# Performance work log

Hardware: AMD Instinct MI355X
Metric: run time of the kernel (lower is better)

## Reference

```python
import jax, jax.numpy as jnp
import numpy as np

D_MODEL = 1024
N_HEADS = 16
HEAD_DIM = D_MODEL // N_HEADS
LENGTHS = np.array([1536, 1024, 1400, 900, 1200, 1300, 1500, 1000])
OFFSETS = np.concatenate([[0], np.cumsum(LENGTHS)]).astype(np.int32)
N_TOT = int(OFFSETS[-1])
LN_EPS = 1e-5


def _pad_meta(offsets):
    # Static (numpy) gather indices: ragged concat [N,D] -> padded [B,Lmax,D]
    offsets = np.asarray(offsets)
    lengths = np.diff(offsets)
    lmax = int(lengths.max())
    tok = np.arange(lmax)[None, :]                      # [1, Lmax]
    valid = tok < lengths[:, None]                      # [B, Lmax] bool
    src = np.where(valid, offsets[:-1, None] + tok, 0)  # [B, Lmax] int
    return src, valid


def setup_inputs() -> dict:
    key = jax.random.key(0)
    ks = jax.random.split(key, 4)
    s = 1.0 / np.sqrt(D_MODEL)
    return {
        "x": jax.random.normal(ks[0], (N_TOT, D_MODEL), jnp.float32),
        "batch_offsets": jnp.asarray(OFFSETS, jnp.int32),
        "in_proj_w": jax.random.normal(ks[1], (3 * D_MODEL, D_MODEL), jnp.float32) * s,
        "in_proj_b": jnp.zeros((3 * D_MODEL,), jnp.float32),
        "out_w": jax.random.normal(ks[2], (D_MODEL, D_MODEL), jnp.float32) * s,
        "out_b": jnp.zeros((D_MODEL,), jnp.float32),
        "ln_g": jnp.ones((D_MODEL,), jnp.float32),
        "ln_b": jnp.zeros((D_MODEL,), jnp.float32),
    }


def reference(x, batch_offsets, in_proj_w, in_proj_b, out_w, out_b, ln_g, ln_b):
    src, valid = _pad_meta(np.asarray(batch_offsets))
    B, L = valid.shape
    vmask = jnp.asarray(valid)
    # deconcat_add_batch_dim: pad to [B, L, D]
    xp = x[src] * vmask[..., None]
    # pre-LayerNorm
    mu = jnp.mean(xp, axis=-1, keepdims=True)
    var = jnp.mean((xp - mu) ** 2, axis=-1, keepdims=True)
    h = (xp - mu) * jax.lax.rsqrt(var + LN_EPS) * ln_g + ln_b
    # fused qkv projection (torch MHA in_proj)
    qkv = h @ in_proj_w.T + in_proj_b                   # [B, L, 3D]
    q, k, v = jnp.split(qkv, 3, axis=-1)
    def heads(t):
        return t.reshape(B, L, N_HEADS, HEAD_DIM).transpose(0, 2, 1, 3)
    q, k, v = heads(q), heads(k), heads(v)              # [B, H, L, hd]
    scores = jnp.einsum("bhqd,bhkd->bhqk", q, k) / np.sqrt(HEAD_DIM)
    scores = jnp.where(vmask[:, None, None, :], scores, -jnp.inf)
    attn = jax.nn.softmax(scores, axis=-1)
    o = jnp.einsum("bhqk,bhkd->bhqd", attn, v)          # [B, H, L, hd]
    o = o.transpose(0, 2, 1, 3).reshape(B, L, D_MODEL)
    o = o @ out_w.T + out_b
    y = xp + o                                          # residual (dropout p=0)
    # remove_batch_dim_and_concat: unpad back to [N, D]
    return y[vmask]
```

## Files before the change

kernel.cpp:

```cpp
#include <hip/hip_runtime.h>
#include <hip/hip_bf16.h>
#include <stdint.h>

#define D_MODEL 1024
#define QKV_LD  3072
#define N_TOT   9860
#define M_PAD   9984
#define LN_EPS  1e-5f

typedef __bf16 bf16_t;
typedef __bf16 bf16x8 __attribute__((ext_vector_type(8)));
typedef float  f32x4  __attribute__((ext_vector_type(4)));
typedef float  f32x16 __attribute__((ext_vector_type(16)));
typedef uint32_t u32x4 __attribute__((ext_vector_type(4)));

__device__ inline unsigned short f2bf(float f) {
  __bf16 h = (__bf16)f;
  return __builtin_bit_cast(unsigned short, h);
}
__device__ inline int imin(int a, int b) { return a < b ? a : b; }

__device__ inline void plswap(uint32_t& a, uint32_t& b) {
  asm("v_permlane32_swap_b32 %0, %1" : "+v"(a), "+v"(b));
}

__device__ inline void gload_lds16(const bf16_t* g, void* l) {
  __builtin_amdgcn_global_load_lds(
      (const __attribute__((address_space(1))) unsigned int*)g,
      (__attribute__((address_space(3))) unsigned int*)l, 16, 0, 0);
}

__global__ __launch_bounds__(256) void cvt_weights(const float* __restrict__ w_in,
                                                   const float* __restrict__ w_out,
                                                   bf16_t* __restrict__ win,
                                                   bf16_t* __restrict__ wout) {
  const int n_in = QKV_LD * D_MODEL / 4;
  int i = blockIdx.x * 256 + threadIdx.x;
  const float* src;
  ushort4* dst;
  int j;
  if (i < n_in) { src = w_in; dst = (ushort4*)win; j = i; }
  else          { src = w_out; dst = (ushort4*)wout; j = i - n_in; }
  float4 v = ((const float4*)src)[j];
  dst[j] = make_ushort4(f2bf(v.x), f2bf(v.y), f2bf(v.z), f2bf(v.w));
}

__global__ __launch_bounds__(256) void ln_kernel(const float* __restrict__ x,
                                                 const float* __restrict__ g,
                                                 const float* __restrict__ b,
                                                 bf16_t* __restrict__ hout) {
  int row = blockIdx.x;
  int t = threadIdx.x;
  if (row >= N_TOT) {
    ((ushort4*)(hout + (size_t)row * D_MODEL))[t] = make_ushort4(0, 0, 0, 0);
    return;
  }
  float4 v = ((const float4*)(x + (size_t)row * D_MODEL))[t];
  float s  = v.x + v.y + v.z + v.w;
  float sq = v.x * v.x + v.y * v.y + v.z * v.z + v.w * v.w;
  #pragma unroll
  for (int off = 1; off < 64; off <<= 1) {
    s  += __shfl_xor(s, off);
    sq += __shfl_xor(sq, off);
  }
  __shared__ float ss[4], ssq[4];
  int wid = t >> 6;
  if ((t & 63) == 0) { ss[wid] = s; ssq[wid] = sq; }
  __syncthreads();
  s  = ss[0] + ss[1] + ss[2] + ss[3];
  sq = ssq[0] + ssq[1] + ssq[2] + ssq[3];
  float mu  = s * (1.0f / 1024.0f);
  float var = sq * (1.0f / 1024.0f) - mu * mu;
  float rs  = rsqrtf(var + LN_EPS);
  float4 gv = ((const float4*)g)[t];
  float4 bv = ((const float4*)b)[t];
  ushort4 o;
  o.x = f2bf((v.x - mu) * rs * gv.x + bv.x);
  o.y = f2bf((v.y - mu) * rs * gv.y + bv.y);
  o.z = f2bf((v.z - mu) * rs * gv.z + bv.z);
  o.w = f2bf((v.w - mu) * rs * gv.w + bv.w);
  ((ushort4*)(hout + (size_t)row * D_MODEL))[t] = o;
}

template<int NCOLS>
__global__ __launch_bounds__(512) void gemm256(const bf16_t* __restrict__ A,
                                               const bf16_t* __restrict__ B,
                                               const float* __restrict__ bias,
                                               bf16_t* __restrict__ Cbf) {
  constexpr int K = 1024, NKT = K / 64;
  constexpr int GX = M_PAD / 256;
  constexpr int NWG = GX * (NCOLS / 256);
  int bid = blockIdx.x;
  {
    constexpr int q = NWG / 8, r = NWG % 8;
    int x = bid & 7, o = bid >> 3;
    bid = (x < r ? x * (q + 1) : r * (q + 1) + (x - r) * q) + o;
  }
  const int tileM = bid % GX;
  const int tileN = bid / GX;
  const int t = threadIdx.x;
  const int lane = t & 63, wid = t >> 6;
  const int wr = wid >> 2, wc = wid & 3;

  __shared__ bf16_t As[2][256 * 64];
  __shared__ bf16_t Bs[2][256 * 64];

  f32x4 acc[8][4];
  #pragma unroll
  for (int m = 0; m < 8; ++m)
    #pragma unroll
    for (int n = 0; n < 4; ++n)
      acc[m][n] = f32x4{0.f, 0.f, 0.f, 0.f};

  const int rowA0 = tileM * 256, rowB0 = tileN * 256;
  const int lrow = lane >> 3;
  const int lch  = lane & 7;

  auto stage = [&](int buf, int kt) {
    const int k0 = kt * 64;
    #pragma unroll
    for (int i = 0; i < 4; ++i) {
      const int r  = wid * 32 + i * 8 + lrow;
      const int sc = lch ^ (r & 7);
      gload_lds16(A + (size_t)(rowA0 + r) * K + k0 + sc * 8,
                  (char*)&As[buf][(wid * 32 + i * 8) * 64]);
      gload_lds16(B + (size_t)(rowB0 + r) * K + k0 + sc * 8,
                  (char*)&Bs[buf][(wid * 32 + i * 8) * 64]);
    }
  };

  stage(0, 0);

  for (int kt = 0; kt < NKT; ++kt) {
    const int cur = kt & 1;
    if (kt + 1 < NKT) {
      stage(cur ^ 1, kt + 1);
      asm volatile("s_waitcnt vmcnt(8)" ::: "memory");
    } else {
      asm volatile("s_waitcnt vmcnt(0)" ::: "memory");
    }
    __builtin_amdgcn_s_barrier();
    __builtin_amdgcn_sched_barrier(0);

    const char* Ab = (const char*)&As[cur][0];
    const char* Bb = (const char*)&Bs[cur][0];

    bf16x8 bfr[4][2];
    #pragma unroll
    for (int n = 0; n < 4; ++n)
      #pragma unroll
      for (int ks = 0; ks < 2; ++ks) {
        int r = wc * 64 + n * 16 + (lane & 15);
        int c = ks * 4 + (lane >> 4);
        bfr[n][ks] = *(const bf16x8*)(Bb + r * 128 + ((c ^ (r & 7)) * 16));
      }
    #pragma unroll
    for (int p = 0; p < 4; ++p) {
      bf16x8 af[2][2];
      #pragma unroll
      for (int mm = 0; mm < 2; ++mm)
        #pragma unroll
        for (int ks = 0; ks < 2; ++ks) {
          int r = wr * 128 + (p * 2 + mm) * 16 + (lane & 15);
          int c = ks * 4 + (lane >> 4);
          af[mm][ks] = *(const bf16x8*)(Ab + r * 128 + ((c ^ (r & 7)) * 16));
        }
      __builtin_amdgcn_s_setprio(1);
      #pragma unroll
      for (int mm = 0; mm < 2; ++mm)
        #pragma unroll
        for (int n = 0; n < 4; ++n)
          #pragma unroll
          for (int ks = 0; ks < 2; ++ks)
            acc[p * 2 + mm][n] =
                __builtin_amdgcn_mfma_f32_16x16x32_bf16(af[mm][ks], bfr[n][ks],
                                                        acc[p * 2 + mm][n], 0, 0, 0);
      __builtin_amdgcn_s_setprio(0);
    }
    __builtin_amdgcn_sched_barrier(0);
    __builtin_amdgcn_s_barrier();
  }

  #pragma unroll
  for (int m = 0; m < 8; ++m) {
    int rb = tileM * 256 + wr * 128 + m * 16 + ((lane >> 4) << 2);
    #pragma unroll
    for (int n = 0; n < 4; ++n) {
      int cb = tileN * 256 + wc * 64 + n * 16 + (lane & 15);
      float bv = bias[cb];
      #pragma unroll
      for (int j = 0; j < 4; ++j)
        Cbf[(size_t)(rb + j) * NCOLS + cb] = (bf16_t)(acc[m][n][j] + bv);
    }
  }
}

template<int NCOLS, bool FINAL>
__global__ __launch_bounds__(256) void gemm_bt(const bf16_t* __restrict__ A,
                                               const bf16_t* __restrict__ B,
                                               const float* __restrict__ bias,
                                               bf16_t* __restrict__ Cbf,
                                               float* __restrict__ Cf,
                                               const float* __restrict__ resid) {
  constexpr int K = 1024;
  constexpr int GX = M_PAD / 128;
  constexpr int NWG = GX * (NCOLS / 128);
  int bid = blockIdx.x;
  bid = (bid & 7) * (NWG / 8) + (bid >> 3);
  const int tileM = bid % GX;
  const int tileN = bid / GX;
  const int t = threadIdx.x;
  const int lane = t & 63, wid = t >> 6;
  const int wr = wid >> 1, wc = wid & 1;

  __shared__ bf16_t Asm[128 * 64];
  __shared__ bf16_t Bsm[128 * 64];

  f32x4 acc[4][4];
  #pragma unroll
  for (int m = 0; m < 4; ++m)
    #pragma unroll
    for (int n = 0; n < 4; ++n)
      acc[m][n] = f32x4{0.f, 0.f, 0.f, 0.f};

  const int rowA0 = tileM * 128, rowB0 = tileN * 128;
  const int lrow = lane >> 3;
  const int lch  = lane & 7;

  for (int kt = 0; kt < K / 64; ++kt) {
    __syncthreads();
    const int k0 = kt * 64;
    #pragma unroll
    for (int i = 0; i < 4; ++i) {
      const int r  = wid * 32 + i * 8 + lrow;
      const int sc = lch ^ (r & 7);
      gload_lds16(A + (size_t)(rowA0 + r) * K + k0 + sc * 8,
                  (char*)Asm + (wid * 32 + i * 8) * 128);
      gload_lds16(B + (size_t)(rowB0 + r) * K + k0 + sc * 8,
                  (char*)Bsm + (wid * 32 + i * 8) * 128);
    }
    __syncthreads();
    #pragma unroll
    for (int ks = 0; ks < 2; ++ks) {
      bf16x8 af[4], bfr[4];
      #pragma unroll
      for (int m = 0; m < 4; ++m) {
        int r = wr * 64 + m * 16 + (lane & 15);
        int c = ks * 4 + (lane >> 4);
        af[m] = *(const bf16x8*)((const char*)Asm + r * 128 + ((c ^ (r & 7)) * 16));
      }
      #pragma unroll
      for (int n = 0; n < 4; ++n) {
        int r = wc * 64 + n * 16 + (lane & 15);
        int c = ks * 4 + (lane >> 4);
        bfr[n] = *(const bf16x8*)((const char*)Bsm + r * 128 + ((c ^ (r & 7)) * 16));
      }
      #pragma unroll
      for (int m = 0; m < 4; ++m)
        #pragma unroll
        for (int n = 0; n < 4; ++n)
          acc[m][n] = __builtin_amdgcn_mfma_f32_16x16x32_bf16(af[m], bfr[n], acc[m][n], 0, 0, 0);
    }
  }

  #pragma unroll
  for (int m = 0; m < 4; ++m) {
    int rb = tileM * 128 + wr * 64 + m * 16 + ((lane >> 4) << 2);
    #pragma unroll
    for (int n = 0; n < 4; ++n) {
      int cb = tileN * 128 + wc * 64 + n * 16 + (lane & 15);
      float bv = bias[cb];
      #pragma unroll
      for (int j = 0; j < 4; ++j) {
        int grow = rb + j;
        float val = acc[m][n][j] + bv;
        if constexpr (FINAL) {
          if (grow < N_TOT) {
            size_t idx = (size_t)grow * NCOLS + cb;
            Cf[idx] = resid[idx] + val;
          }
        } else {
          Cbf[(size_t)grow * NCOLS + cb] = (bf16_t)val;
        }
      }
    }
  }
}

__global__ __launch_bounds__(256) void transpose_v(const bf16_t* __restrict__ qkv,
                                                   bf16_t* __restrict__ vt) {
  static const int OFF_[8] = {0, 1536, 2560, 3960, 4860, 6060, 7360, 8860};
  static const int SH_[8]  = {0, 0, 0, 0, 4, 4, 8, 12};
  __shared__ bf16_t tile[64][72];
  const int t = threadIdx.x;
  const int n0 = blockIdx.x * 64, c0 = blockIdx.y * 64;
  #pragma unroll
  for (int it = 0; it < 2; ++it) {
    int idx = it * 256 + t;
    int row = idx >> 3, ch = idx & 7;
    bf16x8 v = *(const bf16x8*)(qkv + (size_t)(n0 + row) * QKV_LD + 2048 + c0 + ch * 8);
    *(bf16x8*)(&tile[row][ch * 8]) = v;
  }
  __syncthreads();
  #pragma unroll
  for (int it = 0; it < 2; ++it) {
    int idx = it * 256 + t;
    int crow = idx >> 3, ng = idx & 7;
    int tok0 = n0 + ng * 8;
    if (tok0 >= N_TOT) continue;
    bf16x8 o;
    #pragma unroll
    for (int i = 0; i < 8; ++i) o[i] = tile[ng * 8 + i][crow];
    int b0 = 0;
    #pragma unroll
    for (int i = 1; i < 8; ++i) b0 += (tok0 >= OFF_[i]);
    bool fast = (tok0 + 7 < N_TOT);
    if (fast) {
      int b7 = 0;
      #pragma unroll
      for (int i = 1; i < 8; ++i) b7 += (tok0 + 7 >= OFF_[i]);
      fast = (b7 == b0);
    }
    bf16_t* vrow = vt + (size_t)(c0 + crow) * M_PAD;
    if (fast) {
      *(bf16x8*)(vrow + tok0 + SH_[b0]) = o;
    } else {
      #pragma unroll
      for (int i = 0; i < 8; ++i) {
        int tok = tok0 + i;
        if (tok < N_TOT) {
          int bb = 0;
          #pragma unroll
          for (int k = 1; k < 8; ++k) bb += (tok >= OFF_[k]);
          vrow[tok + SH_[bb]] = o[i];
        }
      }
    }
  }
}

__global__ __launch_bounds__(256) void attn_mfma(const bf16_t* __restrict__ qkv,
                                                 const bf16_t* __restrict__ vt,
                                                 bf16_t* __restrict__ obuf) {
  static const int off0_[8] = {0, 7360, 2560, 6060, 4860, 1536, 8860, 3960};
  static const int vcol_[8] = {0, 7368, 2560, 6064, 4864, 1536, 8872, 3960};
  static const int len_[8]  = {1536, 1500, 1400, 1300, 1200, 1024, 1000, 900};
  static const int ts_[9]   = {0, 12, 24, 35, 46, 56, 64, 72, 80};
  const int tt = blockIdx.x;
  const int h  = blockIdx.y;
  int b = 0;
  #pragma unroll
  for (int i = 1; i < 8; ++i) b += (tt >= ts_[i]);
  const int L     = len_[b];
  const int kbase = off0_[b];
  const int vcol  = vcol_[b];
  const int q0    = (tt - ts_[b]) * 128;
  const int tok0  = kbase + q0;
  const int nq    = imin(L - q0, 128);

  const int t = threadIdx.x;
  const int lane = t & 63, w = t >> 6;
  const int qcol = lane & 31, hi = lane >> 5;

  __shared__ char Ks[3][8192];
  __shared__ char Vs[3][8192];

  const float MSHIFT = 16.0f;

  bf16x8 qf[4];
  {
    const bf16_t* qp = qkv + (size_t)(tok0 + w * 32 + qcol) * QKV_LD + h * 64;
    #pragma unroll
    for (int c = 0; c < 4; ++c) {
      bf16x8 v = *(const bf16x8*)(qp + c * 16 + hi * 8);
      #pragma unroll
      for (int i = 0; i < 8; ++i) v[i] = (__bf16)((float)v[i] * 0.125f);
      qf[c] = v;
    }
  }

  f32x16 accO[2];
  #pragma unroll
  for (int db = 0; db < 2; ++db)
    #pragma unroll
    for (int i = 0; i < 16; ++i) accO[db][i] = 0.f;
  float lsum = 0.f;

  const int srow = w * 8 + (lane >> 3);
  const int sch  = lane & 7;
  const int sc   = sch ^ (srow & 7);

  auto stage = [&](int buf, int kv0) {
    #pragma unroll
    for (int it = 0; it < 2; ++it) {
      int row = srow + it * 32;
      gload_lds16(qkv + (size_t)(kbase + kv0 + row) * QKV_LD + 1024 + h * 64 + sc * 8,
                  &Ks[buf][w * 1024 + it * 4096]);
      gload_lds16(vt + (size_t)(h * 64 + row) * M_PAD + vcol + kv0 + sc * 8,
                  &Vs[buf][w * 1024 + it * 4096]);
    }
  };

  const int nt = (L + 63) >> 6;
  stage(0, 0);
  stage(1, 64);
  int cur = 0;

  for (int ti = 0; ti < nt; ++ti) {
    const int nk = imin(L - ti * 64, 64);
    if (ti + 1 < nt) {
      asm volatile("s_waitcnt vmcnt(4)" ::: "memory");
    } else {
      asm volatile("s_waitcnt vmcnt(0)" ::: "memory");
    }
    __builtin_amdgcn_s_barrier();
    __builtin_amdgcn_sched_barrier(0);
    if (ti + 2 < nt) {
      int nbuf = cur + 2; if (nbuf >= 3) nbuf -= 3;
      stage(nbuf, (ti + 2) * 64);
    }

    const char* Kb = Ks[cur];
    const char* Vb = Vs[cur];

    f32x16 accS[2];
    #pragma unroll
    for (int kb = 0; kb < 2; ++kb)
      #pragma unroll
      for (int i = 0; i < 16; ++i) accS[kb][i] = 0.f;
    __builtin_amdgcn_s_setprio(1);
    #pragma unroll
    for (int kb = 0; kb < 2; ++kb) {
      int key = kb * 32 + qcol;
      #pragma unroll
      for (int c = 0; c < 4; ++c) {
        bf16x8 kf = *(const bf16x8*)(Kb + key * 128 + (((2 * c + hi) ^ (key & 7)) * 16));
        accS[kb] = __builtin_amdgcn_mfma_f32_32x32x16_bf16(kf, qf[c], accS[kb], 0, 0, 0);
      }
    }
    __builtin_amdgcn_s_setprio(0);

    if (nk < 64) {
      #pragma unroll
      for (int kb = 0; kb < 2; ++kb)
        #pragma unroll
        for (int r = 0; r < 16; ++r)
          if (kb * 32 + (r & 3) + 8 * (r >> 2) + 4 * hi >= nk) accS[kb][r] = -INFINITY;
    }

    bf16x8 pb[2][2];
    #pragma unroll
    for (int kb = 0; kb < 2; ++kb) {
      uint32_t G[4][2];
      #pragma unroll
      for (int j = 0; j < 4; ++j) {
        float p0 = __expf(accS[kb][4 * j + 0] - MSHIFT);
        float p1 = __expf(accS[kb][4 * j + 1] - MSHIFT);
        float p2 = __expf(accS[kb][4 * j + 2] - MSHIFT);
        float p3 = __expf(accS[kb][4 * j + 3] - MSHIFT);
        lsum += (p0 + p1) + (p2 + p3);
        G[j][0] = (uint32_t)f2bf(p0) | ((uint32_t)f2bf(p1) << 16);
        G[j][1] = (uint32_t)f2bf(p2) | ((uint32_t)f2bf(p3) << 16);
      }
      #pragma unroll
      for (int c = 0; c < 2; ++c) {
        uint32_t ax = G[2 * c][0], bx = G[2 * c + 1][0];
        uint32_t ay = G[2 * c][1], by = G[2 * c + 1][1];
        plswap(ax, bx);
        plswap(ay, by);
        u32x4 u; u[0] = ax; u[1] = ay; u[2] = bx; u[3] = by;
        pb[kb][c] = __builtin_bit_cast(bf16x8, u);
      }
    }

    __builtin_amdgcn_s_setprio(1);
    #pragma unroll
    for (int kb = 0; kb < 2; ++kb)
      #pragma unroll
      for (int c = 0; c < 2; ++c) {
        int ch = 4 * kb + 2 * c + hi;
        #pragma unroll
        for (int db = 0; db < 2; ++db) {
          int dim = db * 32 + qcol;
          bf16x8 vf = *(const bf16x8*)(Vb + dim * 128 + ((ch ^ (dim & 7)) * 16));
          accO[db] = __builtin_amdgcn_mfma_f32_32x32x16_bf16(vf, pb[kb][c], accO[db], 0, 0, 0);
        }
      }
    __builtin_amdgcn_s_setprio(0);
    cur = (cur == 2) ? 0 : cur + 1;
  }

  float l = lsum + __shfl_xor(lsum, 32);
  const int qlocal = w * 32 + qcol;
  if (qlocal < nq) {
    float inv = 1.f / l;
    bf16_t* op = obuf + (size_t)(tok0 + qlocal) * D_MODEL + h * 64;
    #pragma unroll
    for (int db = 0; db < 2; ++db)
      #pragma unroll
      for (int rr = 0; rr < 4; ++rr) {
        float v0 = accO[db][4 * rr + 0] * inv;
        float v1 = accO[db][4 * rr + 1] * inv;
        float v2 = accO[db][4 * rr + 2] * inv;
        float v3 = accO[db][4 * rr + 3] * inv;
        uint2 u;
        u.x = (uint32_t)f2bf(v0) | ((uint32_t)f2bf(v1) << 16);
        u.y = (uint32_t)f2bf(v2) | ((uint32_t)f2bf(v3) << 16);
        *(uint2*)(op + db * 32 + rr * 8 + hi * 4) = u;
      }
  }
}

extern "C" void kernel_launch(void* const* d_in, const int* in_sizes, int n_in,
                              void* d_out, int out_size, void* d_ws, size_t ws_size,
                              hipStream_t stream) {
  const float* x     = (const float*)d_in[0];
  const float* w_in  = (const float*)d_in[2];
  const float* b_in  = (const float*)d_in[3];
  const float* w_out = (const float*)d_in[4];
  const float* b_out = (const float*)d_in[5];
  const float* ln_g  = (const float*)d_in[6];
  const float* ln_b  = (const float*)d_in[7];
  float* out = (float*)d_out;

  char* ws = (char*)d_ws;
  const size_t SZ_H   = (size_t)M_PAD * D_MODEL * 2;
  const size_t SZ_QKV = (size_t)M_PAD * QKV_LD * 2;
  const size_t SZ_O   = SZ_H;
  const size_t SZ_WIN = (size_t)QKV_LD * D_MODEL * 2;
  const size_t SZ_WO  = (size_t)D_MODEL * D_MODEL * 2;
  if (ws_size < SZ_H + SZ_QKV + SZ_O + SZ_WIN + SZ_WO) return;

  bf16_t* h_bf    = (bf16_t*)ws;
  bf16_t* qkv_bf  = (bf16_t*)(ws + SZ_H);
  bf16_t* o_bf    = (bf16_t*)(ws + SZ_H + SZ_QKV);
  bf16_t* win_bf  = (bf16_t*)(ws + SZ_H + SZ_QKV + SZ_O);
  bf16_t* wout_bf = (bf16_t*)(ws + SZ_H + SZ_QKV + SZ_O + SZ_WIN);

  cvt_weights<<<(QKV_LD * D_MODEL / 4 + D_MODEL * D_MODEL / 4) / 256, 256, 0, stream>>>(
      w_in, w_out, win_bf, wout_bf);

  ln_kernel<<<M_PAD, 256, 0, stream>>>(x, ln_g, ln_b, h_bf);

  gemm256<QKV_LD><<<(M_PAD / 256) * (QKV_LD / 256), 512, 0, stream>>>(
      h_bf, win_bf, b_in, qkv_bf);

  bf16_t* vt = h_bf;
  transpose_v<<<dim3(M_PAD / 64, D_MODEL / 64), 256, 0, stream>>>(qkv_bf, vt);

  attn_mfma<<<dim3(80, 16), 256, 0, stream>>>(qkv_bf, vt, o_bf);

  gemm_bt<D_MODEL, true><<<(M_PAD / 128) * (D_MODEL / 128), 256, 0, stream>>>(
      o_bf, wout_bf, b_out, nullptr, out, x);
}
```

Baseline: 300.9 us.

## Fuse V transpose into QKV GEMM epilogue and merge weight cvt into LN

```diff
diff --git a/kernel.cpp b/kernel.cpp
--- a/kernel.cpp
+++ b/kernel.cpp
@@ -30,27 +30,28 @@
       (__attribute__((address_space(3))) unsigned int*)l, 16, 0, 0);
 }
 
-__global__ __launch_bounds__(256) void cvt_weights(const float* __restrict__ w_in,
-                                                   const float* __restrict__ w_out,
-                                                   bf16_t* __restrict__ win,
-                                                   bf16_t* __restrict__ wout) {
-  const int n_in = QKV_LD * D_MODEL / 4;
-  int i = blockIdx.x * 256 + threadIdx.x;
-  const float* src;
-  ushort4* dst;
-  int j;
-  if (i < n_in) { src = w_in; dst = (ushort4*)win; j = i; }
-  else          { src = w_out; dst = (ushort4*)wout; j = i - n_in; }
-  float4 v = ((const float4*)src)[j];
-  dst[j] = make_ushort4(f2bf(v.x), f2bf(v.y), f2bf(v.z), f2bf(v.w));
-}
-
-__global__ __launch_bounds__(256) void ln_kernel(const float* __restrict__ x,
-                                                 const float* __restrict__ g,
-                                                 const float* __restrict__ b,
-                                                 bf16_t* __restrict__ hout) {
+__global__ __launch_bounds__(256) void ln_cvt_kernel(const float* __restrict__ x,
+                                                     const float* __restrict__ g,
+                                                     const float* __restrict__ b,
+                                                     bf16_t* __restrict__ hout,
+                                                     const float* __restrict__ w_in,
+                                                     const float* __restrict__ w_out,
+                                                     bf16_t* __restrict__ win,
+                                                     bf16_t* __restrict__ wout) {
   int row = blockIdx.x;
   int t = threadIdx.x;
+  if (row >= M_PAD) {
+    const int n_in = QKV_LD * D_MODEL / 4;
+    int i = (row - M_PAD) * 256 + t;
+    const float* src;
+    ushort4* dst;
+    int j;
+    if (i < n_in) { src = w_in; dst = (ushort4*)win; j = i; }
+    else          { src = w_out; dst = (ushort4*)wout; j = i - n_in; }
+    float4 v = ((const float4*)src)[j];
+    dst[j] = make_ushort4(f2bf(v.x), f2bf(v.y), f2bf(v.z), f2bf(v.w));
+    return;
+  }
   if (row >= N_TOT) {
     ((ushort4*)(hout + (size_t)row * D_MODEL))[t] = make_ushort4(0, 0, 0, 0);
     return;
@@ -82,11 +83,12 @@
   ((ushort4*)(hout + (size_t)row * D_MODEL))[t] = o;
 }
 
-template<int NCOLS>
+template<int NCOLS, bool VT>
 __global__ __launch_bounds__(512) void gemm256(const bf16_t* __restrict__ A,
                                                const bf16_t* __restrict__ B,
                                                const float* __restrict__ bias,
-                                               bf16_t* __restrict__ Cbf) {
+                                               bf16_t* __restrict__ Cbf,
+                                               bf16_t* __restrict__ vt) {
   constexpr int K = 1024, NKT = K / 64;
   constexpr int GX = M_PAD / 256;
   constexpr int NWG = GX * (NCOLS / 256);
@@ -181,16 +183,41 @@
     __builtin_amdgcn_s_barrier();
   }
 
-  #pragma unroll
-  for (int m = 0; m < 8; ++m) {
-    int rb = tileM * 256 + wr * 128 + m * 16 + ((lane >> 4) << 2);
-    #pragma unroll
-    for (int n = 0; n < 4; ++n) {
-      int cb = tileN * 256 + wc * 64 + n * 16 + (lane & 15);
-      float bv = bias[cb];
-      #pragma unroll
-      for (int j = 0; j < 4; ++j)
-        Cbf[(size_t)(rb + j) * NCOLS + cb] = (bf16_t)(acc[m][n][j] + bv);
+  if (VT && tileN >= 8) {
+    static const int OFF_[8] = {0, 1536, 2560, 3960, 4860, 6060, 7360, 8860};
+    static const int SH_[8]  = {0, 0, 0, 0, 4, 4, 8, 12};
+    #pragma unroll
+    for (int m = 0; m < 8; ++m) {
+      int rb = tileM * 256 + wr * 128 + m * 16 + ((lane >> 4) << 2);
+      if (rb >= N_TOT) continue;
+      int bb = 0;
+      #pragma unroll
+      for (int i = 1; i < 8; ++i) bb += (rb >= OFF_[i]);
+      int col0 = rb + SH_[bb];
+      #pragma unroll
+      for (int n = 0; n < 4; ++n) {
+        int cb = tileN * 256 + wc * 64 + n * 16 + (lane & 15);
+        float bv = bias[cb];
+        float v0 = acc[m][n][0] + bv, v1 = acc[m][n][1] + bv;
+        float v2 = acc[m][n][2] + bv, v3 = acc[m][n][3] + bv;
+        uint2 u;
+        u.x = (uint32_t)f2bf(v0) | ((uint32_t)f2bf(v1) << 16);
+        u.y = (uint32_t)f2bf(v2) | ((uint32_t)f2bf(v3) << 16);
+        *(uint2*)(vt + (size_t)(cb - 2048) * M_PAD + col0) = u;
+      }
+    }
+  } else {
+    #pragma unroll
+    for (int m = 0; m < 8; ++m) {
+      int rb = tileM * 256 + wr * 128 + m * 16 + ((lane >> 4) << 2);
+      #pragma unroll
+      for (int n = 0; n < 4; ++n) {
+        int cb = tileN * 256 + wc * 64 + n * 16 + (lane & 15);
+        float bv = bias[cb];
+        #pragma unroll
+        for (int j = 0; j < 4; ++j)
+          Cbf[(size_t)(rb + j) * NCOLS + cb] = (bf16_t)(acc[m][n][j] + bv);
+      }
     }
   }
 }
@@ -281,58 +308,6 @@
           }
         } else {
           Cbf[(size_t)grow * NCOLS + cb] = (bf16_t)val;
-        }
-      }
-    }
-  }
-}
-
-__global__ __launch_bounds__(256) void transpose_v(const bf16_t* __restrict__ qkv,
-                                                   bf16_t* __restrict__ vt) {
-  static const int OFF_[8] = {0, 1536, 2560, 3960, 4860, 6060, 7360, 8860};
-  static const int SH_[8]  = {0, 0, 0, 0, 4, 4, 8, 12};
-  __shared__ bf16_t tile[64][72];
-  const int t = threadIdx.x;
-  const int n0 = blockIdx.x * 64, c0 = blockIdx.y * 64;
-  #pragma unroll
-  for (int it = 0; it < 2; ++it) {
-    int idx = it * 256 + t;
-    int row = idx >> 3, ch = idx & 7;
-    bf16x8 v = *(const bf16x8*)(qkv + (size_t)(n0 + row) * QKV_LD + 2048 + c0 + ch * 8);
-    *(bf16x8*)(&tile[row][ch * 8]) = v;
-  }
-  __syncthreads();
-  #pragma unroll
-  for (int it = 0; it < 2; ++it) {
-    int idx = it * 256 + t;
-    int crow = idx >> 3, ng = idx & 7;
-    int tok0 = n0 + ng * 8;
-    if (tok0 >= N_TOT) continue;
-    bf16x8 o;
-    #pragma unroll
-    for (int i = 0; i < 8; ++i) o[i] = tile[ng * 8 + i][crow];
-    int b0 = 0;
-    #pragma unroll
-    for (int i = 1; i < 8; ++i) b0 += (tok0 >= OFF_[i]);
-    bool fast = (tok0 + 7 < N_TOT);
-    if (fast) {
-      int b7 = 0;
-      #pragma unroll
-      for (int i = 1; i < 8; ++i) b7 += (tok0 + 7 >= OFF_[i]);
-      fast = (b7 == b0);
-    }
-    bf16_t* vrow = vt + (size_t)(c0 + crow) * M_PAD;
-    if (fast) {
-      *(bf16x8*)(vrow + tok0 + SH_[b0]) = o;
-    } else {
-      #pragma unroll
-      for (int i = 0; i < 8; ++i) {
-        int tok = tok0 + i;
-        if (tok < N_TOT) {
-          int bb = 0;
-          #pragma unroll
-          for (int k = 1; k < 8; ++k) bb += (tok >= OFF_[k]);
-          vrow[tok + SH_[bb]] = o[i];
         }
       }
     }
@@ -529,24 +504,22 @@
   const size_t SZ_O   = SZ_H;
   const size_t SZ_WIN = (size_t)QKV_LD * D_MODEL * 2;
   const size_t SZ_WO  = (size_t)D_MODEL * D_MODEL * 2;
-  if (ws_size < SZ_H + SZ_QKV + SZ_O + SZ_WIN + SZ_WO) return;
+  const size_t SZ_VT  = SZ_H;
+  if (ws_size < SZ_H + SZ_QKV + SZ_O + SZ_WIN + SZ_WO + SZ_VT) return;
 
   bf16_t* h_bf    = (bf16_t*)ws;
   bf16_t* qkv_bf  = (bf16_t*)(ws + SZ_H);
   bf16_t* o_bf    = (bf16_t*)(ws + SZ_H + SZ_QKV);
   bf16_t* win_bf  = (bf16_t*)(ws + SZ_H + SZ_QKV + SZ_O);
   bf16_t* wout_bf = (bf16_t*)(ws + SZ_H + SZ_QKV + SZ_O + SZ_WIN);
-
-  cvt_weights<<<(QKV_LD * D_MODEL / 4 + D_MODEL * D_MODEL / 4) / 256, 256, 0, stream>>>(
-      w_in, w_out, win_bf, wout_bf);
-
-  ln_kernel<<<M_PAD, 256, 0, stream>>>(x, ln_g, ln_b, h_bf);
-
-  gemm256<QKV_LD><<<(M_PAD / 256) * (QKV_LD / 256), 512, 0, stream>>>(
-      h_bf, win_bf, b_in, qkv_bf);
-
-  bf16_t* vt = h_bf;
-  transpose_v<<<dim3(M_PAD / 64, D_MODEL / 64), 256, 0, stream>>>(qkv_bf, vt);
+  bf16_t* vt      = (bf16_t*)(ws + SZ_H + SZ_QKV + SZ_O + SZ_WIN + SZ_WO);
+
+  const int cvt_blocks = (QKV_LD * D_MODEL / 4 + D_MODEL * D_MODEL / 4) / 256;
+  ln_cvt_kernel<<<M_PAD + cvt_blocks, 256, 0, stream>>>(
+      x, ln_g, ln_b, h_bf, w_in, w_out, win_bf, wout_bf);
+
+  gemm256<QKV_LD, true><<<(M_PAD / 256) * (QKV_LD / 256), 512, 0, stream>>>(
+      h_bf, win_bf, b_in, qkv_bf, vt);
 
   attn_mfma<<<dim3(80, 16), 256, 0, stream>>>(qkv_bf, vt, o_bf);
 
```

Result: no change. 297.3 us (-1.2%).
